# Kernel optimization log

Hardware: AMD Instinct MI355X
Metric: run time of the kernel (lower is better)

## Reference

```python
import jax, jax.numpy as jnp
import numpy as np
import math

N = 100000   # outputSize (memory bank rows)
D = 128      # inputSize (feature dim)
B = 128      # batch size
K = 4096     # number of negatives per sample
T = 0.07     # temperature
MOMENTUM = 0.5


def setup_inputs() -> dict:
    key = jax.random.key(0)
    k1, k2, k3, k4, k5 = jax.random.split(key, 5)
    stdv = 1.0 / math.sqrt(D / 3.0)
    # l2-normalized features, as produced by the encoder in contrastive setups
    v1 = jax.random.normal(k1, (B, D), dtype=jnp.float32)
    v1 = v1 / jnp.linalg.norm(v1, axis=1, keepdims=True)
    v2 = jax.random.normal(k2, (B, D), dtype=jnp.float32)
    v2 = v2 / jnp.linalg.norm(v2, axis=1, keepdims=True)
    idx = jax.random.randint(k3, (B, K + 1), 0, N, dtype=jnp.int32)  # pos+neg bank rows
    y = jnp.arange(B, dtype=jnp.int32)  # distinct positive slots (first-visit behavior)
    # memory buffers initialized U(-stdv, stdv), as in torch.rand*2*stdv - stdv
    memory_v1 = jax.random.uniform(k4, (N, D), dtype=jnp.float32, minval=-stdv, maxval=stdv)
    memory_v2 = jax.random.uniform(k5, (N, D), dtype=jnp.float32, minval=-stdv, maxval=stdv)
    return {"v1": v1, "v2": v2, "idx": idx, "y": y,
            "memory_v1": memory_v1, "memory_v2": memory_v2}


def reference(v1, v2, idx, y, memory_v1, memory_v2):
    n_out = memory_v1.shape[0]
    # gather K+1 rows per sample (detached in the original -> stop_gradient)
    w1 = jax.lax.stop_gradient(memory_v1[idx])  # [B, K+1, D]
    w2 = jax.lax.stop_gradient(memory_v2[idx])  # [B, K+1, D]
    # batched vector-matrix product + exp/T
    out_v2 = jnp.exp(jnp.einsum('bkd,bd->bk', w1, v2) / T)  # [B, K+1]
    out_v1 = jnp.exp(jnp.einsum('bkd,bd->bk', w2, v1) / T)  # [B, K+1]
    # normalization constants (first-call Z computation: mean * outputSize)
    Z_v1 = jax.lax.stop_gradient(out_v1.mean()) * n_out
    Z_v2 = jax.lax.stop_gradient(out_v2.mean()) * n_out
    out_v1 = out_v1 / Z_v1
    out_v2 = out_v2 / Z_v2
    # momentum-blended normalize-and-scatter memory update (no_grad in torch)
    upd1 = MOMENTUM * memory_v1[y] + (1.0 - MOMENTUM) * v1  # [B, D]
    upd1 = upd1 / jnp.linalg.norm(upd1, axis=1, keepdims=True)
    new_memory_v1 = memory_v1.at[y].set(upd1)
    upd2 = MOMENTUM * memory_v2[y] + (1.0 - MOMENTUM) * v2
    upd2 = upd2 / jnp.linalg.norm(upd2, axis=1, keepdims=True)
    new_memory_v2 = memory_v2.at[y].set(upd2)
    return out_v1, out_v2, new_memory_v1, new_memory_v2
```

## Files before the change

kernel.cpp:

```cpp
#include <hip/hip_runtime.h>
#include <math.h>

constexpr int N_ROWS = 100000;
constexpr int D      = 128;
constexpr int B      = 128;
constexpr int KP1    = 4097;
constexpr int TOTAL_PAIRS = B * KP1;
constexpr float INV_T = 1.0f / 0.07f;
constexpr int N4 = N_ROWS * (D / 4);

constexpr int SC_BLOCKS = 2048;
constexpr int CP_BLOCKS = 2048;

typedef float fvec4 __attribute__((ext_vector_type(4)));

__global__ void init_ws_kernel(float* ws) {
    if (threadIdx.x < 2) ws[threadIdx.x] = 0.0f;
}

__device__ __forceinline__ float dot4(float4 a, float4 b) {
    return a.x * b.x + a.y * b.y + a.z * b.z + a.w * b.w;
}

__device__ __forceinline__ float red32(float v) {
    #pragma unroll
    for (int off = 16; off >= 1; off >>= 1) v += __shfl_xor(v, off);
    return v;
}

__global__ __launch_bounds__(256) void score_kernel(
    const float* __restrict__ v1, const float* __restrict__ v2,
    const int* __restrict__ idx,
    const float* __restrict__ mem1, const float* __restrict__ mem2,
    float* __restrict__ out,
    float* __restrict__ sums)
{
    __shared__ alignas(16) int s_idx[260];
    __shared__ float s1[8], s2[8];

    const int sid   = blockIdx.x;
    const int tid   = threadIdx.x;
    const int l     = tid & 31;
    const int grp   = tid >> 5;
    const int b     = sid >> 4;
    const int chunk = sid & 15;
    const int cnt   = (chunk == 15) ? 257 : 256;
    const int ibase = b * KP1 + chunk * 256;

    for (int t = tid; t < cnt; t += 256) s_idx[t] = idx[ibase + t];
    __syncthreads();

    const float4* __restrict__ m1 = (const float4*)mem1;
    const float4* __restrict__ m2 = (const float4*)mem2;
    const float4 a1 = ((const float4*)v1)[b * 32 + l];
    const float4 a2 = ((const float4*)v2)[b * 32 + l];

    const int lk    = grp * 32;
    const int pbase = ibase + lk;

    float acc1 = 0.0f, acc2 = 0.0f;

    for (int u = 0; u < 32; u += 4) {
        const int4 rr = *(const int4*)&s_idx[lk + u];

        float4 wA0 = m2[(size_t)rr.x * 32 + l];
        float4 wB0 = m1[(size_t)rr.x * 32 + l];
        float4 wA1 = m2[(size_t)rr.y * 32 + l];
        float4 wB1 = m1[(size_t)rr.y * 32 + l];
        float4 wA2 = m2[(size_t)rr.z * 32 + l];
        float4 wB2 = m1[(size_t)rr.z * 32 + l];
        float4 wA3 = m2[(size_t)rr.w * 32 + l];
        float4 wB3 = m1[(size_t)rr.w * 32 + l];

        float dA0 = red32(dot4(wA0, a1));
        float dB0 = red32(dot4(wB0, a2));
        float dA1 = red32(dot4(wA1, a1));
        float dB1 = red32(dot4(wB1, a2));
        float dA2 = red32(dot4(wA2, a1));
        float dB2 = red32(dot4(wB2, a2));
        float dA3 = red32(dot4(wA3, a1));
        float dB3 = red32(dot4(wB3, a2));

        float eA0 = __expf(dA0 * INV_T);
        float eB0 = __expf(dB0 * INV_T);
        float eA1 = __expf(dA1 * INV_T);
        float eB1 = __expf(dB1 * INV_T);
        float eA2 = __expf(dA2 * INV_T);
        float eB2 = __expf(dB2 * INV_T);
        float eA3 = __expf(dA3 * INV_T);
        float eB3 = __expf(dB3 * INV_T);

        acc1 += (eA0 + eA1) + (eA2 + eA3);
        acc2 += (eB0 + eB1) + (eB2 + eB3);

        float sa  = (l & 1) ? eA1 : eA0;
        float sb  = (l & 1) ? eA3 : eA2;
        float evA = (l & 2) ? sb : sa;
        float sc  = (l & 1) ? eB1 : eB0;
        float sd  = (l & 1) ? eB3 : eB2;
        float evB = (l & 2) ? sd : sc;
        int p = pbase + u;
        if (l < 4)      out[p + l] = evA;
        else if (l < 8) out[TOTAL_PAIRS + p + (l - 4)] = evB;
    }

    if (chunk == 15 && grp == 7) {
        int r = s_idx[256];
        float4 wA = m2[(size_t)r * 32 + l];
        float4 wB = m1[(size_t)r * 32 + l];
        float dA = red32(dot4(wA, a1));
        float dB = red32(dot4(wB, a2));
        float eA = __expf(dA * INV_T);
        float eB = __expf(dB * INV_T);
        acc1 += eA;
        acc2 += eB;
        if (l == 0) {
            out[b * KP1 + 4096]               = eA;
            out[TOTAL_PAIRS + b * KP1 + 4096] = eB;
        }
    }

    if (l == 0) { s1[grp] = acc1; s2[grp] = acc2; }
    __syncthreads();
    if (tid == 0) {
        float t1 = 0.0f, t2 = 0.0f;
        #pragma unroll
        for (int i = 0; i < 8; ++i) { t1 += s1[i]; t2 += s2[i]; }
        atomicAdd(&sums[0], t1);
        atomicAdd(&sums[1], t2);
    }
}

__global__ __launch_bounds__(256) void copy_scale_kernel(
    const float* __restrict__ mem1, const float* __restrict__ mem2,
    float* __restrict__ o1, float* __restrict__ o2,
    float* __restrict__ out, const float* __restrict__ sums)
{
    const fvec4* __restrict__ m1 = (const fvec4*)mem1;
    const fvec4* __restrict__ m2 = (const fvec4*)mem2;
    fvec4* __restrict__ d1 = (fvec4*)o1;
    fvec4* __restrict__ d2 = (fvec4*)o2;

    int tid    = blockIdx.x * 256 + threadIdx.x;
    int stride = CP_BLOCKS * 256;
    for (int i = tid; i < N4; i += stride) {
        fvec4 x1 = m1[i];
        fvec4 x2 = m2[i];
        __builtin_nontemporal_store(x1, &d1[i]);
        __builtin_nontemporal_store(x2, &d2[i]);
    }

    float sc1 = (float)((double)TOTAL_PAIRS / ((double)sums[0] * (double)N_ROWS));
    float sc2 = (float)((double)TOTAL_PAIRS / ((double)sums[1] * (double)N_ROWS));
    for (int i = tid; i < 2 * TOTAL_PAIRS; i += stride) {
        out[i] *= (i < TOTAL_PAIRS) ? sc1 : sc2;
    }
}

__global__ void rowupd_kernel(
    const float* __restrict__ v1, const float* __restrict__ v2,
    const int* __restrict__ y,
    const float* __restrict__ mem1, const float* __restrict__ mem2,
    float* __restrict__ o1, float* __restrict__ o2)
{
    int b    = blockIdx.x & (B - 1);
    int bank = blockIdx.x >> 7;
    int lane = threadIdx.x;
    const float2* __restrict__ m = (const float2*)(bank ? mem2 : mem1);
    const float2* __restrict__ v = (const float2*)(bank ? v2 : v1);
    float2* __restrict__ o       = (float2*)(bank ? o2 : o1);
    int row = y[b];
    float2 mv = m[(size_t)row * 64 + lane];
    float2 vv = v[b * 64 + lane];
    float2 u;
    u.x = 0.5f * mv.x + 0.5f * vv.x;
    u.y = 0.5f * mv.y + 0.5f * vv.y;
    float ss = u.x * u.x + u.y * u.y;
    #pragma unroll
    for (int off = 32; off >= 1; off >>= 1) ss += __shfl_xor(ss, off);
    float inv = 1.0f / sqrtf(ss);
    float2 r; r.x = u.x * inv; r.y = u.y * inv;
    o[(size_t)row * 64 + lane] = r;
}

extern "C" void kernel_launch(void* const* d_in, const int* in_sizes, int n_in,
                              void* d_out, int out_size, void* d_ws, size_t ws_size,
                              hipStream_t stream) {
    const float* v1   = (const float*)d_in[0];
    const float* v2   = (const float*)d_in[1];
    const int*   idx  = (const int*)d_in[2];
    const int*   y    = (const int*)d_in[3];
    const float* mem1 = (const float*)d_in[4];
    const float* mem2 = (const float*)d_in[5];

    float* out = (float*)d_out;
    float* out_mem1 = out + 2 * (size_t)TOTAL_PAIRS;
    float* out_mem2 = out_mem1 + (size_t)N_ROWS * D;
    float* sums = (float*)d_ws;

    init_ws_kernel<<<1, 64, 0, stream>>>(sums);

    score_kernel<<<SC_BLOCKS, 256, 0, stream>>>(
        v1, v2, idx, mem1, mem2, out, sums);

    copy_scale_kernel<<<CP_BLOCKS, 256, 0, stream>>>(
        mem1, mem2, out_mem1, out_mem2, out, sums);

    rowupd_kernel<<<2 * B, 64, 0, stream>>>(
        v1, v2, y, mem1, mem2, out_mem1, out_mem2);
}
```

Before: 286.8 us.

## Process gathered memory rows in address-range passes for cache locality

The score kernel now visits each warp's 32 gathered rows in eight passes over disjoint row-index ranges, using a ballot to pick the rows that fall in the current range. The aim is to keep all blocks touching a similar slice of the memory banks at the same moment so the gathers hit in L2/MALL rather than going to HBM. Results are staged in shared memory and written out coalesced, with the sum reduction done afterwards. In exchange the inner loop has fewer independent loads in flight (two rows instead of four), extra ballot and shuffle work per pass, and nothing keeps blocks actually in step across ranges.

Measured after the change: 287.2 us. No clear change (+0.1%).

```diff
diff --git a/kernel.cpp b/kernel.cpp
--- a/kernel.cpp
+++ b/kernel.cpp
@@ -12,6 +12,9 @@
 constexpr int SC_BLOCKS = 2048;
 constexpr int CP_BLOCKS = 2048;
 
+constexpr int NRANGE = 8;
+constexpr int RSPAN  = N_ROWS / NRANGE;
+
 typedef float fvec4 __attribute__((ext_vector_type(4)));
 
 __global__ void init_ws_kernel(float* ws) {
@@ -35,8 +38,8 @@
     float* __restrict__ out,
     float* __restrict__ sums)
 {
-    __shared__ alignas(16) int s_idx[260];
-    __shared__ float s1[8], s2[8];
+    __shared__ float s_e1[260], s_e2[260];
+    __shared__ float s_p1[4], s_p2[4];
 
     const int sid   = blockIdx.x;
     const int tid   = threadIdx.x;
@@ -46,86 +49,78 @@
     const int chunk = sid & 15;
     const int cnt   = (chunk == 15) ? 257 : 256;
     const int ibase = b * KP1 + chunk * 256;
-
-    for (int t = tid; t < cnt; t += 256) s_idx[t] = idx[ibase + t];
-    __syncthreads();
+    const int lk    = grp * 32;
 
     const float4* __restrict__ m1 = (const float4*)mem1;
     const float4* __restrict__ m2 = (const float4*)mem2;
     const float4 a1 = ((const float4*)v1)[b * 32 + l];
     const float4 a2 = ((const float4*)v2)[b * 32 + l];
 
-    const int lk    = grp * 32;
-    const int pbase = ibase + lk;
-
-    float acc1 = 0.0f, acc2 = 0.0f;
-
-    for (int u = 0; u < 32; u += 4) {
-        const int4 rr = *(const int4*)&s_idx[lk + u];
-
-        float4 wA0 = m2[(size_t)rr.x * 32 + l];
-        float4 wB0 = m1[(size_t)rr.x * 32 + l];
-        float4 wA1 = m2[(size_t)rr.y * 32 + l];
-        float4 wB1 = m1[(size_t)rr.y * 32 + l];
-        float4 wA2 = m2[(size_t)rr.z * 32 + l];
-        float4 wB2 = m1[(size_t)rr.z * 32 + l];
-        float4 wA3 = m2[(size_t)rr.w * 32 + l];
-        float4 wB3 = m1[(size_t)rr.w * 32 + l];
-
-        float dA0 = red32(dot4(wA0, a1));
-        float dB0 = red32(dot4(wB0, a2));
-        float dA1 = red32(dot4(wA1, a1));
-        float dB1 = red32(dot4(wB1, a2));
-        float dA2 = red32(dot4(wA2, a1));
-        float dB2 = red32(dot4(wB2, a2));
-        float dA3 = red32(dot4(wA3, a1));
-        float dB3 = red32(dot4(wB3, a2));
-
-        float eA0 = __expf(dA0 * INV_T);
-        float eB0 = __expf(dB0 * INV_T);
-        float eA1 = __expf(dA1 * INV_T);
-        float eB1 = __expf(dB1 * INV_T);
-        float eA2 = __expf(dA2 * INV_T);
-        float eB2 = __expf(dB2 * INV_T);
-        float eA3 = __expf(dA3 * INV_T);
-        float eB3 = __expf(dB3 * INV_T);
-
-        acc1 += (eA0 + eA1) + (eA2 + eA3);
-        acc2 += (eB0 + eB1) + (eB2 + eB3);
-
-        float sa  = (l & 1) ? eA1 : eA0;
-        float sb  = (l & 1) ? eA3 : eA2;
-        float evA = (l & 2) ? sb : sa;
-        float sc  = (l & 1) ? eB1 : eB0;
-        float sd  = (l & 1) ? eB3 : eB2;
-        float evB = (l & 2) ? sd : sc;
-        int p = pbase + u;
-        if (l < 4)      out[p + l] = evA;
-        else if (l < 8) out[TOTAL_PAIRS + p + (l - 4)] = evB;
-    }
-
-    if (chunk == 15 && grp == 7) {
-        int r = s_idx[256];
-        float4 wA = m2[(size_t)r * 32 + l];
-        float4 wB = m1[(size_t)r * 32 + l];
-        float dA = red32(dot4(wA, a1));
-        float dB = red32(dot4(wB, a2));
-        float eA = __expf(dA * INV_T);
-        float eB = __expf(dB * INV_T);
-        acc1 += eA;
-        acc2 += eB;
-        if (l == 0) {
-            out[b * KP1 + 4096]               = eA;
-            out[TOTAL_PAIRS + b * KP1 + 4096] = eB;
+    const int  row_l    = idx[ibase + lk + l];
+    const bool has_tail = (chunk == 15) && (grp == 7);
+    const int  row_t    = has_tail ? idx[b * KP1 + 4096] : 0;
+
+    for (int r = 0; r < NRANGE; ++r) {
+        const int lo = r * RSPAN;
+        const int hi = lo + RSPAN;
+
+        unsigned long long bal = __ballot(row_l >= lo && row_l < hi);
+        unsigned mask = (tid & 32) ? (unsigned)(bal >> 32) : (unsigned)bal;
+
+        while (mask) {
+            int j0 = __builtin_ctz(mask); mask &= mask - 1;
+            int r0 = __shfl(row_l, j0, 32);
+            float4 wA0 = m2[(size_t)r0 * 32 + l];
+            float4 wB0 = m1[(size_t)r0 * 32 + l];
+
+            int j1 = -1;
+            float4 wA1{}, wB1{};
+            if (mask) {
+                j1 = __builtin_ctz(mask); mask &= mask - 1;
+                int r1 = __shfl(row_l, j1, 32);
+                wA1 = m2[(size_t)r1 * 32 + l];
+                wB1 = m1[(size_t)r1 * 32 + l];
+            }
+
+            float eA0 = __expf(red32(dot4(wA0, a1)) * INV_T);
+            float eB0 = __expf(red32(dot4(wB0, a2)) * INV_T);
+            if (l == 0) { s_e1[lk + j0] = eA0; s_e2[lk + j0] = eB0; }
+
+            if (j1 >= 0) {
+                float eA1 = __expf(red32(dot4(wA1, a1)) * INV_T);
+                float eB1 = __expf(red32(dot4(wB1, a2)) * INV_T);
+                if (l == 0) { s_e1[lk + j1] = eA1; s_e2[lk + j1] = eB1; }
+            }
         }
-    }
-
-    if (l == 0) { s1[grp] = acc1; s2[grp] = acc2; }
+
+        if (has_tail && row_t >= lo && row_t < hi) {
+            float4 wA = m2[(size_t)row_t * 32 + l];
+            float4 wB = m1[(size_t)row_t * 32 + l];
+            float eA = __expf(red32(dot4(wA, a1)) * INV_T);
+            float eB = __expf(red32(dot4(wB, a2)) * INV_T);
+            if (l == 0) { s_e1[256] = eA; s_e2[256] = eB; }
+        }
+    }
+    __syncthreads();
+
+    float p1 = 0.0f, p2 = 0.0f;
+    for (int t = tid; t < cnt; t += 256) {
+        float e1 = s_e1[t], e2 = s_e2[t];
+        out[ibase + t]               = e1;
+        out[TOTAL_PAIRS + ibase + t] = e2;
+        p1 += e1; p2 += e2;
+    }
+    #pragma unroll
+    for (int off = 32; off >= 1; off >>= 1) {
+        p1 += __shfl_xor(p1, off);
+        p2 += __shfl_xor(p2, off);
+    }
+    int w = tid >> 6;
+    if ((tid & 63) == 0) { s_p1[w] = p1; s_p2[w] = p2; }
     __syncthreads();
     if (tid == 0) {
-        float t1 = 0.0f, t2 = 0.0f;
-        #pragma unroll
-        for (int i = 0; i < 8; ++i) { t1 += s1[i]; t2 += s2[i]; }
+        float t1 = s_p1[0] + s_p1[1] + s_p1[2] + s_p1[3];
+        float t2 = s_p2[0] + s_p2[1] + s_p2[2] + s_p2[3];
         atomicAdd(&sums[0], t1);
         atomicAdd(&sums[1], t2);
     }
```

## Invert gather into row-major pass via counting sort, fusing score with memory copy

Applied to the files above, without the earlier changes.

Builds a per-bank-row list of (sample,negative) pairs with histogram, prefix scan and scatter kernels, then one fused kernel streams each memory row once. That row pass writes the copy and computes all of the row's dot products against the cached v1/v2 rows, so the random gather that rereads memory rows is avoided. The cost is several extra small launches, atomics, workspace traffic for the pair list, and scattered single-lane output writes. It needs a large workspace and falls back to the old path if the workspace is too small.

After: 349.3 us. +21.8%, slower.

```diff
diff --git a/kernel.cpp b/kernel.cpp
--- a/kernel.cpp
+++ b/kernel.cpp
@@ -9,35 +9,218 @@
 constexpr float INV_T = 1.0f / 0.07f;
 constexpr int N4 = N_ROWS * (D / 4);
 
-constexpr int SC_BLOCKS = 2048;
-constexpr int CP_BLOCKS = 2048;
+constexpr int SCAN_BLOCKS = (N_ROWS + 255) / 256;
+constexpr int FUSE_BLOCKS = 2048;
+constexpr int NGROUPS     = FUSE_BLOCKS * 8;
+
+constexpr size_t WS_OFFS   = 16;
+constexpr size_t WS_CURSOR = WS_OFFS + (size_t)N_ROWS * 4;
+constexpr size_t WS_BTOT   = WS_CURSOR + (size_t)N_ROWS * 4;
+constexpr size_t WS_PLIST  = WS_BTOT + 512 * 4;
+constexpr size_t WS_NEEDED = WS_PLIST + (size_t)TOTAL_PAIRS * 4;
 
 typedef float fvec4 __attribute__((ext_vector_type(4)));
-
-__global__ void init_ws_kernel(float* ws) {
-    if (threadIdx.x < 2) ws[threadIdx.x] = 0.0f;
-}
 
 __device__ __forceinline__ float dot4(float4 a, float4 b) {
     return a.x * b.x + a.y * b.y + a.z * b.z + a.w * b.w;
 }
-
 __device__ __forceinline__ float red32(float v) {
     #pragma unroll
     for (int off = 16; off >= 1; off >>= 1) v += __shfl_xor(v, off);
     return v;
 }
 
+__global__ __launch_bounds__(256) void zero_ws_kernel(float* sums, int* offs) {
+    int i = blockIdx.x * 256 + threadIdx.x;
+    if (i < 2) sums[i] = 0.0f;
+    for (int j = i; j < N_ROWS; j += gridDim.x * 256) offs[j] = 0;
+}
+
+__global__ __launch_bounds__(256) void hist_kernel(
+    const int* __restrict__ idx, int* __restrict__ offs) {
+    int stride = gridDim.x * 256;
+    for (int p = blockIdx.x * 256 + threadIdx.x; p < TOTAL_PAIRS; p += stride)
+        atomicAdd(&offs[idx[p]], 1);
+}
+
+__global__ __launch_bounds__(256) void scan_block_kernel(
+    int* __restrict__ offs, int* __restrict__ btot) {
+    __shared__ int buf[256];
+    const int t = threadIdx.x;
+    const int i = blockIdx.x * 256 + t;
+    int v = (i < N_ROWS) ? offs[i] : 0;
+    buf[t] = v;
+    __syncthreads();
+    for (int off = 1; off < 256; off <<= 1) {
+        int y = (t >= off) ? buf[t - off] : 0;
+        __syncthreads();
+        buf[t] += y;
+        __syncthreads();
+    }
+    if (i < N_ROWS) offs[i] = buf[t] - v;
+    if (t == 255) btot[blockIdx.x] = buf[t];
+}
+
+__global__ void scan_btot_kernel(int* __restrict__ btot) {
+    __shared__ int buf[512];
+    const int t = threadIdx.x;
+    int v = (t < SCAN_BLOCKS) ? btot[t] : 0;
+    buf[t] = v;
+    __syncthreads();
+    for (int off = 1; off < 512; off <<= 1) {
+        int y = (t >= off) ? buf[t - off] : 0;
+        __syncthreads();
+        buf[t] += y;
+        __syncthreads();
+    }
+    if (t < SCAN_BLOCKS) btot[t] = buf[t] - v;
+}
+
+__global__ __launch_bounds__(256) void addback_kernel(
+    int* __restrict__ offs, const int* __restrict__ btot, int* __restrict__ cursor) {
+    int i = blockIdx.x * 256 + threadIdx.x;
+    if (i < N_ROWS) {
+        int o = offs[i] + btot[i >> 8];
+        offs[i] = o;
+        cursor[i] = o;
+    }
+}
+
+__global__ __launch_bounds__(256) void scatter_kernel(
+    const int* __restrict__ idx, int* __restrict__ cursor, int* __restrict__ plist) {
+    int stride = gridDim.x * 256;
+    for (int p = blockIdx.x * 256 + threadIdx.x; p < TOTAL_PAIRS; p += stride) {
+        int r = idx[p];
+        int pos = atomicAdd(&cursor[r], 1);
+        plist[pos] = p;
+    }
+}
+
+__global__ __launch_bounds__(256) void fused_kernel(
+    const float* __restrict__ v1, const float* __restrict__ v2,
+    const float* __restrict__ mem1, const float* __restrict__ mem2,
+    const int* __restrict__ offs, const int* __restrict__ cend,
+    const int* __restrict__ plist,
+    float* __restrict__ out, float* __restrict__ sums,
+    float* __restrict__ o1, float* __restrict__ o2)
+{
+    __shared__ float s1[8], s2[8];
+    const int tid = threadIdx.x;
+    const int l   = tid & 31;
+    const int grp = tid >> 5;
+    const int g   = blockIdx.x * 8 + grp;
+
+    const float4* __restrict__ m1 = (const float4*)mem1;
+    const float4* __restrict__ m2 = (const float4*)mem2;
+    const float4* __restrict__ V1 = (const float4*)v1;
+    const float4* __restrict__ V2 = (const float4*)v2;
+    fvec4* __restrict__ d1 = (fvec4*)o1;
+    fvec4* __restrict__ d2 = (fvec4*)o2;
+
+    float acc1 = 0.0f, acc2 = 0.0f;
+
+    for (int r = g; r < N_ROWS; r += NGROUPS) {
+        float4 w1 = m1[(size_t)r * 32 + l];
+        float4 w2 = m2[(size_t)r * 32 + l];
+
+        fvec4 x1 = {w1.x, w1.y, w1.z, w1.w};
+        fvec4 x2 = {w2.x, w2.y, w2.z, w2.w};
+        __builtin_nontemporal_store(x1, &d1[(size_t)r * 32 + l]);
+        __builtin_nontemporal_store(x2, &d2[(size_t)r * 32 + l]);
+
+        int q = offs[r];
+        const int e = cend[r];
+        for (; q + 1 < e; q += 2) {
+            int p0 = plist[q], p1 = plist[q + 1];
+            int b0 = p0 / KP1, b1 = p1 / KP1;
+            float4 a10 = V1[b0 * 32 + l], a20 = V2[b0 * 32 + l];
+            float4 a11 = V1[b1 * 32 + l], a21 = V2[b1 * 32 + l];
+            float dA0 = red32(dot4(w2, a10));
+            float dB0 = red32(dot4(w1, a20));
+            float dA1 = red32(dot4(w2, a11));
+            float dB1 = red32(dot4(w1, a21));
+            float eA0 = __expf(dA0 * INV_T), eB0 = __expf(dB0 * INV_T);
+            float eA1 = __expf(dA1 * INV_T), eB1 = __expf(dB1 * INV_T);
+            acc1 += eA0 + eA1;
+            acc2 += eB0 + eB1;
+            if (l == 0) {
+                out[p0] = eA0; out[TOTAL_PAIRS + p0] = eB0;
+                out[p1] = eA1; out[TOTAL_PAIRS + p1] = eB1;
+            }
+        }
+        if (q < e) {
+            int p0 = plist[q];
+            int b0 = p0 / KP1;
+            float4 a10 = V1[b0 * 32 + l], a20 = V2[b0 * 32 + l];
+            float dA0 = red32(dot4(w2, a10));
+            float dB0 = red32(dot4(w1, a20));
+            float eA0 = __expf(dA0 * INV_T), eB0 = __expf(dB0 * INV_T);
+            acc1 += eA0;
+            acc2 += eB0;
+            if (l == 0) { out[p0] = eA0; out[TOTAL_PAIRS + p0] = eB0; }
+        }
+    }
+
+    if (l == 0) { s1[grp] = acc1; s2[grp] = acc2; }
+    __syncthreads();
+    if (tid == 0) {
+        float t1 = 0.0f, t2 = 0.0f;
+        #pragma unroll
+        for (int i = 0; i < 8; ++i) { t1 += s1[i]; t2 += s2[i]; }
+        atomicAdd(&sums[0], t1);
+        atomicAdd(&sums[1], t2);
+    }
+}
+
+__global__ __launch_bounds__(256) void finish_kernel(
+    float* __restrict__ out, const float* __restrict__ sums,
+    const float* __restrict__ v1, const float* __restrict__ v2,
+    const int* __restrict__ y,
+    const float* __restrict__ mem1, const float* __restrict__ mem2,
+    float* __restrict__ o1, float* __restrict__ o2)
+{
+    if (blockIdx.x < 2 * B && threadIdx.x < 64) {
+        int b    = blockIdx.x & (B - 1);
+        int bank = blockIdx.x >> 7;
+        int lane = threadIdx.x;
+        const float2* __restrict__ m = (const float2*)(bank ? mem2 : mem1);
+        const float2* __restrict__ v = (const float2*)(bank ? v2 : v1);
+        float2* __restrict__ o       = (float2*)(bank ? o2 : o1);
+        int row = y[b];
+        float2 mv = m[(size_t)row * 64 + lane];
+        float2 vv = v[b * 64 + lane];
+        float2 u;
+        u.x = 0.5f * mv.x + 0.5f * vv.x;
+        u.y = 0.5f * mv.y + 0.5f * vv.y;
+        float ss = u.x * u.x + u.y * u.y;
+        #pragma unroll
+        for (int off = 32; off >= 1; off >>= 1) ss += __shfl_xor(ss, off);
+        float inv = 1.0f / sqrtf(ss);
+        float2 r; r.x = u.x * inv; r.y = u.y * inv;
+        o[(size_t)row * 64 + lane] = r;
+    }
+
+    float sc1 = (float)((double)TOTAL_PAIRS / ((double)sums[0] * (double)N_ROWS));
+    float sc2 = (float)((double)TOTAL_PAIRS / ((double)sums[1] * (double)N_ROWS));
+    int stride = gridDim.x * blockDim.x;
+    for (int i = blockIdx.x * blockDim.x + threadIdx.x; i < 2 * TOTAL_PAIRS;
+         i += stride) {
+        out[i] *= (i < TOTAL_PAIRS) ? sc1 : sc2;
+    }
+}
+
+__global__ void init_ws_kernel(float* ws) {
+    if (threadIdx.x < 2) ws[threadIdx.x] = 0.0f;
+}
+
 __global__ __launch_bounds__(256) void score_kernel(
     const float* __restrict__ v1, const float* __restrict__ v2,
     const int* __restrict__ idx,
     const float* __restrict__ mem1, const float* __restrict__ mem2,
-    float* __restrict__ out,
-    float* __restrict__ sums)
+    float* __restrict__ out, float* __restrict__ sums)
 {
     __shared__ alignas(16) int s_idx[260];
     __shared__ float s1[8], s2[8];
-
     const int sid   = blockIdx.x;
     const int tid   = threadIdx.x;
     const int l     = tid & 31;
@@ -46,80 +229,49 @@
     const int chunk = sid & 15;
     const int cnt   = (chunk == 15) ? 257 : 256;
     const int ibase = b * KP1 + chunk * 256;
-
     for (int t = tid; t < cnt; t += 256) s_idx[t] = idx[ibase + t];
     __syncthreads();
-
     const float4* __restrict__ m1 = (const float4*)mem1;
     const float4* __restrict__ m2 = (const float4*)mem2;
     const float4 a1 = ((const float4*)v1)[b * 32 + l];
     const float4 a2 = ((const float4*)v2)[b * 32 + l];
-
-    const int lk    = grp * 32;
-    const int pbase = ibase + lk;
-
+    const int lk = grp * 32, pbase = ibase + lk;
     float acc1 = 0.0f, acc2 = 0.0f;
-
     for (int u = 0; u < 32; u += 4) {
         const int4 rr = *(const int4*)&s_idx[lk + u];
-
-        float4 wA0 = m2[(size_t)rr.x * 32 + l];
-        float4 wB0 = m1[(size_t)rr.x * 32 + l];
-        float4 wA1 = m2[(size_t)rr.y * 32 + l];
-        float4 wB1 = m1[(size_t)rr.y * 32 + l];
-        float4 wA2 = m2[(size_t)rr.z * 32 + l];
-        float4 wB2 = m1[(size_t)rr.z * 32 + l];
-        float4 wA3 = m2[(size_t)rr.w * 32 + l];
-        float4 wB3 = m1[(size_t)rr.w * 32 + l];
-
-        float dA0 = red32(dot4(wA0, a1));
-        float dB0 = red32(dot4(wB0, a2));
-        float dA1 = red32(dot4(wA1, a1));
-        float dB1 = red32(dot4(wB1, a2));
-        float dA2 = red32(dot4(wA2, a1));
-        float dB2 = red32(dot4(wB2, a2));
-        float dA3 = red32(dot4(wA3, a1));
-        float dB3 = red32(dot4(wB3, a2));
-
-        float eA0 = __expf(dA0 * INV_T);
-        float eB0 = __expf(dB0 * INV_T);
-        float eA1 = __expf(dA1 * INV_T);
-        float eB1 = __expf(dB1 * INV_T);
-        float eA2 = __expf(dA2 * INV_T);
-        float eB2 = __expf(dB2 * INV_T);
-        float eA3 = __expf(dA3 * INV_T);
-        float eB3 = __expf(dB3 * INV_T);
-
+        float4 wA0 = m2[(size_t)rr.x * 32 + l], wB0 = m1[(size_t)rr.x * 32 + l];
+        float4 wA1 = m2[(size_t)rr.y * 32 + l], wB1 = m1[(size_t)rr.y * 32 + l];
+        float4 wA2 = m2[(size_t)rr.z * 32 + l], wB2 = m1[(size_t)rr.z * 32 + l];
+        float4 wA3 = m2[(size_t)rr.w * 32 + l], wB3 = m1[(size_t)rr.w * 32 + l];
+        float eA0 = __expf(red32(dot4(wA0, a1)) * INV_T);
+        float eB0 = __expf(red32(dot4(wB0, a2)) * INV_T);
+        float eA1 = __expf(red32(dot4(wA1, a1)) * INV_T);
+        float eB1 = __expf(red32(dot4(wB1, a2)) * INV_T);
+        float eA2 = __expf(red32(dot4(wA2, a1)) * INV_T);
+        float eB2 = __expf(red32(dot4(wB2, a2)) * INV_T);
+        float eA3 = __expf(red32(dot4(wA3, a1)) * INV_T);
+        float eB3 = __expf(red32(dot4(wB3, a2)) * INV_T);
         acc1 += (eA0 + eA1) + (eA2 + eA3);
         acc2 += (eB0 + eB1) + (eB2 + eB3);
-
-        float sa  = (l & 1) ? eA1 : eA0;
-        float sb  = (l & 1) ? eA3 : eA2;
+        float sa = (l & 1) ? eA1 : eA0, sb = (l & 1) ? eA3 : eA2;
         float evA = (l & 2) ? sb : sa;
-        float sc  = (l & 1) ? eB1 : eB0;
-        float sd  = (l & 1) ? eB3 : eB2;
+        float sc = (l & 1) ? eB1 : eB0, sd = (l & 1) ? eB3 : eB2;
         float evB = (l & 2) ? sd : sc;
         int p = pbase + u;
         if (l < 4)      out[p + l] = evA;
         else if (l < 8) out[TOTAL_PAIRS + p + (l - 4)] = evB;
     }
-
     if (chunk == 15 && grp == 7) {
         int r = s_idx[256];
-        float4 wA = m2[(size_t)r * 32 + l];
-        float4 wB = m1[(size_t)r * 32 + l];
-        float dA = red32(dot4(wA, a1));
-        float dB = red32(dot4(wB, a2));
-        float eA = __expf(dA * INV_T);
-        float eB = __expf(dB * INV_T);
-        acc1 += eA;
-        acc2 += eB;
+        float4 wA = m2[(size_t)r * 32 + l], wB = m1[(size_t)r * 32 + l];
+        float eA = __expf(red32(dot4(wA, a1)) * INV_T);
+        float eB = __expf(red32(dot4(wB, a2)) * INV_T);
+        acc1 += eA; acc2 += eB;
         if (l == 0) {
-            out[b * KP1 + 4096]               = eA;
+            out[b * KP1 + 4096] = eA;
             out[TOTAL_PAIRS + b * KP1 + 4096] = eB;
         }
     }
-
     if (l == 0) { s1[grp] = acc1; s2[grp] = acc2; }
     __syncthreads();
     if (tid == 0) {
@@ -140,16 +292,13 @@
     const fvec4* __restrict__ m2 = (const fvec4*)mem2;
     fvec4* __restrict__ d1 = (fvec4*)o1;
     fvec4* __restrict__ d2 = (fvec4*)o2;
-
-    int tid    = blockIdx.x * 256 + threadIdx.x;
-    int stride = CP_BLOCKS * 256;
+    int tid = blockIdx.x * 256 + threadIdx.x;
+    int stride = gridDim.x * 256;
     for (int i = tid; i < N4; i += stride) {
-        fvec4 x1 = m1[i];
-        fvec4 x2 = m2[i];
+        fvec4 x1 = m1[i], x2 = m2[i];
         __builtin_nontemporal_store(x1, &d1[i]);
         __builtin_nontemporal_store(x2, &d2[i]);
     }
-
     float sc1 = (float)((double)TOTAL_PAIRS / ((double)sums[0] * (double)N_ROWS));
     float sc2 = (float)((double)TOTAL_PAIRS / ((double)sums[1] * (double)N_ROWS));
     for (int i = tid; i < 2 * TOTAL_PAIRS; i += stride) {
@@ -196,16 +345,33 @@
     float* out = (float*)d_out;
     float* out_mem1 = out + 2 * (size_t)TOTAL_PAIRS;
     float* out_mem2 = out_mem1 + (size_t)N_ROWS * D;
+    char*  ws   = (char*)d_ws;
     float* sums = (float*)d_ws;
 
-    init_ws_kernel<<<1, 64, 0, stream>>>(sums);
-
-    score_kernel<<<SC_BLOCKS, 256, 0, stream>>>(
-        v1, v2, idx, mem1, mem2, out, sums);
-
-    copy_scale_kernel<<<CP_BLOCKS, 256, 0, stream>>>(
-        mem1, mem2, out_mem1, out_mem2, out, sums);
-
-    rowupd_kernel<<<2 * B, 64, 0, stream>>>(
-        v1, v2, y, mem1, mem2, out_mem1, out_mem2);
-}
+    if (ws_size >= WS_NEEDED) {
+        int* offs   = (int*)(ws + WS_OFFS);
+        int* cursor = (int*)(ws + WS_CURSOR);
+        int* btot   = (int*)(ws + WS_BTOT);
+        int* plist  = (int*)(ws + WS_PLIST);
+
+        zero_ws_kernel<<<256, 256, 0, stream>>>(sums, offs);
+        hist_kernel<<<512, 256, 0, stream>>>(idx, offs);
+        scan_block_kernel<<<SCAN_BLOCKS, 256, 0, stream>>>(offs, btot);
+        scan_btot_kernel<<<1, 512, 0, stream>>>(btot);
+        addback_kernel<<<SCAN_BLOCKS, 256, 0, stream>>>(offs, btot, cursor);
+        scatter_kernel<<<512, 256, 0, stream>>>(idx, cursor, plist);
+        fused_kernel<<<FUSE_BLOCKS, 256, 0, stream>>>(
+            v1, v2, mem1, mem2, offs, cursor, plist,
+            out, sums, out_mem1, out_mem2);
+        finish_kernel<<<1024, 256, 0, stream>>>(
+            out, sums, v1, v2, y, mem1, mem2, out_mem1, out_mem2);
+    } else {
+        init_ws_kernel<<<1, 64, 0, stream>>>(sums);
+        score_kernel<<<2048, 256, 0, stream>>>(
+            v1, v2, idx, mem1, mem2, out, sums);
+        copy_scale_kernel<<<2048, 256, 0, stream>>>(
+            mem1, mem2, out_mem1, out_mem2, out, sums);
+        rowupd_kernel<<<2 * B, 64, 0, stream>>>(
+            v1, v2, y, mem1, mem2, out_mem1, out_mem2);
+    }
+}
```
